# Kernel optimization log

Hardware: AMD Instinct MI355X
Metric: run time of the kernel (lower is better)

The kernel has to match this reference:

```python
import jax, jax.numpy as jnp
import numpy as np

NUM_HEADS = 4
NUM_GROUPS = 32
EPS = 1e-6


def group_norm(x, gamma, beta):
    # x: [b, c, h, w]
    b, c, h, w = x.shape
    xg = x.reshape(b, NUM_GROUPS, c // NUM_GROUPS, h, w)
    mu = xg.mean(axis=(2, 3, 4), keepdims=True)
    var = xg.var(axis=(2, 3, 4), keepdims=True)
    xn = ((xg - mu) * jax.lax.rsqrt(var + EPS)).reshape(b, c, h, w)
    return xn * gamma[None, :, None, None] + beta[None, :, None, None]


def conv1x1(x, W, b):
    # 1x1 conv == per-pixel channel matmul. W: [out_c, in_c], b: [out_c]
    return jnp.einsum('bchw,oc->bohw', x, W) + b[None, :, None, None]


def setup_inputs() -> dict:
    key = jax.random.key(0)
    ks = jax.random.split(key, 8)
    c = 256
    b, h, w = 1, 64, 64
    s = 1.0 / np.sqrt(c)
    return {
        'x_kv': jax.random.normal(ks[0], (b, c, h, w), dtype=jnp.float32),
        'gn_gamma': jnp.ones((c,), dtype=jnp.float32),
        'gn_beta': jnp.zeros((c,), dtype=jnp.float32),
        'Wq': jax.random.normal(ks[1], (c, c), dtype=jnp.float32) * s,
        'bq': jnp.zeros((c,), dtype=jnp.float32),
        'Wk': jax.random.normal(ks[2], (c, c), dtype=jnp.float32) * s,
        'bk': jnp.zeros((c,), dtype=jnp.float32),
        'Wv': jax.random.normal(ks[3], (c, c), dtype=jnp.float32) * s,
        'bv': jnp.zeros((c,), dtype=jnp.float32),
        'Wp': jax.random.normal(ks[4], (c, c), dtype=jnp.float32) * s,
        'bp': jnp.zeros((c,), dtype=jnp.float32),
    }


def reference(x_kv, gn_gamma, gn_beta, Wq, bq, Wk, bk, Wv, bv, Wp, bp):
    b, c, h, w = x_kv.shape
    hd = c // NUM_HEADS
    n = h * w

    h_norm = group_norm(x_kv, gn_gamma, gn_beta)  # self-attn: same norm for q,k,v

    q = conv1x1(h_norm, Wq, bq).reshape(b, NUM_HEADS, hd, n).transpose(0, 1, 3, 2)  # [b,H,n,hd]
    k = conv1x1(h_norm, Wk, bk).reshape(b, NUM_HEADS, hd, n)                        # [b,H,hd,n]
    v = conv1x1(h_norm, Wv, bv).reshape(b, NUM_HEADS, hd, n).transpose(0, 1, 3, 2)  # [b,H,n,hd]

    scores = jnp.einsum('bhnd,bhdm->bhnm', q, k) * (hd ** -0.5)  # [b,H,n,n]
    attn = jax.nn.softmax(scores, axis=-1)
    out = jnp.einsum('bhnm,bhmd->bhnd', attn, v)  # [b,H,n,hd]

    # Faithful to torch: permute(0,2,1,3).contiguous().view(b,c,h,w)
    out = out.transpose(0, 2, 1, 3).reshape(b, c, h, w)
    return x_kv + conv1x1(out, Wp, bp)
```

## Files before the change

### kernel.cpp

```cpp
#include <hip/hip_runtime.h>
#include <hip/hip_bf16.h>

#define NPIX 4096
#define CCH  256
#define HD   64
#define GSIZE 32768

typedef __bf16 bf16x8 __attribute__((ext_vector_type(8)));
typedef __bf16 bf16x4 __attribute__((ext_vector_type(4)));
typedef float  f32x4  __attribute__((ext_vector_type(4)));

#define XPITCH 264


__global__ __launch_bounds__(256) void stats_wconv(
    const float* __restrict__ X,
    const float* __restrict__ Wq, const float* __restrict__ Wk,
    const float* __restrict__ Wv, const float* __restrict__ Wp,
    float* __restrict__ psum, float* __restrict__ pssq, __bf16* __restrict__ Wb)
{
    const int bid = blockIdx.x, t = threadIdx.x;
    if (bid < 256) {
        const float* base = X + bid * 4096;
        float sum = 0.f, ssq = 0.f;
        #pragma unroll
        for (int k = 0; k < 4; ++k) {
            float4 v = *(const float4*)(base + t * 4 + k * 1024);
            sum += v.x + v.y + v.z + v.w;
            ssq += v.x * v.x + v.y * v.y + v.z * v.z + v.w * v.w;
        }
        #pragma unroll
        for (int off = 1; off < 64; off <<= 1) {
            sum += __shfl_xor(sum, off);
            ssq += __shfl_xor(ssq, off);
        }
        __shared__ float red[2][4];
        const int wv = t >> 6;
        if ((t & 63) == 0) { red[0][wv] = sum; red[1][wv] = ssq; }
        __syncthreads();
        if (t == 0) {
            psum[bid] = red[0][0] + red[0][1] + red[0][2] + red[0][3];
            pssq[bid] = red[1][0] + red[1][1] + red[1][2] + red[1][3];
        }
    } else {
        const int j0 = (bid - 256) * 4096 + t * 16;
        const int m  = j0 >> 16;
        const float* W = (m == 0) ? Wq : (m == 1) ? Wk : (m == 2) ? Wv : Wp;
        const float sc = (m == 0) ? 0.125f : 1.f;
        const int off = j0 & 65535;
        #pragma unroll
        for (int k = 0; k < 4; ++k) {
            float4 v = *(const float4*)(W + off + k * 4);
            bf16x4 o;
            o[0] = (__bf16)(v.x * sc); o[1] = (__bf16)(v.y * sc);
            o[2] = (__bf16)(v.z * sc); o[3] = (__bf16)(v.w * sc);
            *(bf16x4*)(Wb + m * 65536 + off + k * 4) = o;
        }
    }
}

__global__ __launch_bounds__(256) void gn_qkv(
    const float* __restrict__ X, const float* __restrict__ gamma,
    const float* __restrict__ beta,
    const float* __restrict__ psum, const float* __restrict__ pssq,
    const __bf16* __restrict__ Wb,
    const float* __restrict__ bq, const float* __restrict__ bk,
    const float* __restrict__ bv,
    __bf16* __restrict__ Qb, __bf16* __restrict__ Kb, __bf16* __restrict__ Vb)
{
    __shared__ __bf16 tile[64 * XPITCH];
    __shared__ float al[256], bl[256];

    const int t = threadIdx.x, lane = t & 63, wave = t >> 6;
    const int l16 = lane & 15, quad = lane >> 4;
    const int p0 = blockIdx.x * 64;
    const int z = blockIdx.y >> 1, och = blockIdx.y & 1;

    {
        const int g = t >> 3;
        float s = 0.f, q = 0.f;
        #pragma unroll
        for (int j = 0; j < 8; ++j) { s += psum[g * 8 + j]; q += pssq[g * 8 + j]; }
        const float mu  = s * (1.f / GSIZE);
        const float var = q * (1.f / GSIZE) - mu * mu;
        const float a = gamma[t] * rsqrtf(var + 1e-6f);
        al[t] = a;
        bl[t] = beta[t] - mu * a;
    }
    __syncthreads();

    #pragma unroll 4
    for (int i = 0; i < 16; ++i) {
        const int c4 = wave * 64 + i * 4;
        f32x4 a4 = *(const f32x4*)(al + c4);
        f32x4 b4 = *(const f32x4*)(bl + c4);
        bf16x4 pk;
        pk[0] = (__bf16)(X[(c4 + 0) * NPIX + p0 + lane] * a4[0] + b4[0]);
        pk[1] = (__bf16)(X[(c4 + 1) * NPIX + p0 + lane] * a4[1] + b4[1]);
        pk[2] = (__bf16)(X[(c4 + 2) * NPIX + p0 + lane] * a4[2] + b4[2]);
        pk[3] = (__bf16)(X[(c4 + 3) * NPIX + p0 + lane] * a4[3] + b4[3]);
        *(bf16x4*)(tile + lane * XPITCH + c4) = pk;
    }
    __syncthreads();

    const int pw = wave * 16;
    bf16x8 xf[8];
    #pragma unroll
    for (int kc = 0; kc < 8; ++kc)
        xf[kc] = *(const bf16x8*)(tile + (pw + l16) * XPITCH + kc * 32 + quad * 8);

    const __bf16* Wz = Wb + z * 65536;
    const float* bias = (z == 0) ? bq : (z == 1) ? bk : bv;

    if (z < 2) {
        const float qs = (z == 0) ? 0.125f : 1.f;
        __bf16* dst = (z == 0) ? Qb : Kb;
        #pragma unroll
        for (int grp = 0; grp < 2; ++grp) {
            f32x4 acc[4] = {};
            #pragma unroll
            for (int kc = 0; kc < 8; ++kc) {
                #pragma unroll
                for (int u = 0; u < 4; ++u) {
                    bf16x8 wf = *(const bf16x8*)(Wz + (och * 128 + (grp * 4 + u) * 16 + l16) * CCH + kc * 32 + quad * 8);
                    acc[u] = __builtin_amdgcn_mfma_f32_16x16x32_bf16(wf, xf[kc], acc[u], 0, 0, 0);
                }
            }
            #pragma unroll
            for (int u = 0; u < 4; ++u) {
                const int ot = och * 8 + grp * 4 + u;
                f32x4 bz = *(const f32x4*)(bias + och * 128 + (grp * 4 + u) * 16 + quad * 4);
                bf16x4 o;
                o[0] = (__bf16)(acc[u][0] + bz[0] * qs);
                o[1] = (__bf16)(acc[u][1] + bz[1] * qs);
                o[2] = (__bf16)(acc[u][2] + bz[2] * qs);
                o[3] = (__bf16)(acc[u][3] + bz[3] * qs);
                const int head = ot >> 2, dloc = (ot & 3) * 16 + quad * 4;
                *(bf16x4*)(dst + head * (NPIX * HD) + (p0 + pw + l16) * HD + dloc) = o;
            }
        }
    } else {
        #pragma unroll
        for (int grp = 0; grp < 2; ++grp) {
            f32x4 acc[4] = {};
            #pragma unroll
            for (int kc = 0; kc < 8; ++kc) {
                #pragma unroll
                for (int u = 0; u < 4; ++u) {
                    bf16x8 wf = *(const bf16x8*)(Wz + (och * 128 + (grp * 4 + u) * 16 + l16) * CCH + kc * 32 + quad * 8);
                    acc[u] = __builtin_amdgcn_mfma_f32_16x16x32_bf16(xf[kc], wf, acc[u], 0, 0, 0);
                }
            }
            #pragma unroll
            for (int u = 0; u < 4; ++u) {
                const int oc = och * 128 + (grp * 4 + u) * 16 + l16;
                const float bz = bias[oc];
                bf16x4 o;
                o[0] = (__bf16)(acc[u][0] + bz); o[1] = (__bf16)(acc[u][1] + bz);
                o[2] = (__bf16)(acc[u][2] + bz); o[3] = (__bf16)(acc[u][3] + bz);
                *(bf16x4*)(Vb + oc * NPIX + p0 + pw + quad * 4) = o;
            }
        }
    }
}

#define KPITCH 72
#define VPITCH 136
#define PPIT   40
#define KBUF   (128 * KPITCH)
#define VBUF   (64 * VPITCH)
#define OFF_K  0
#define OFF_V  (2 * KBUF * 2)
#define OFF_P  (OFF_V + 2 * VBUF * 2)
#define SMEMSZ (OFF_P + 4 * 64 * PPIT * 2)

__global__ __launch_bounds__(256, 1) void attn_mfma(
    const __bf16* __restrict__ Qb, const __bf16* __restrict__ Kb,
    const __bf16* __restrict__ Vb, __bf16* __restrict__ Sb)
{
    __shared__ __align__(16) char smem[SMEMSZ];
    __bf16* ktls = (__bf16*)(smem + OFF_K);
    __bf16* vtls = (__bf16*)(smem + OFF_V);
    __bf16* ptls = (__bf16*)(smem + OFF_P);
    float*  co   = (float*)smem;
    float*  cl   = (float*)(smem + 69632);

    const int t = threadIdx.x, lane = t & 63, wave = t >> 6;
    const int l16 = lane & 15, quad = lane >> 4;

    const int bid  = blockIdx.x;
    const int head = (bid & 7) >> 1;
    const int qt   = ((bid >> 3) << 1) | (bid & 1);
    const int p0   = qt * 64;

    const __bf16* Qh = Qb + head * (NPIX * HD);
    const __bf16* Kh = Kb + head * (NPIX * HD);
    const __bf16* Vh = Vb + head * (HD * NPIX);

    bf16x8 qf[4][2];
    #pragma unroll
    for (int rt = 0; rt < 4; ++rt) {
        const __bf16* qp = Qh + (p0 + rt * 16 + l16) * HD + quad * 8;
        qf[rt][0] = *(const bf16x8*)(qp);
        qf[rt][1] = *(const bf16x8*)(qp + 32);
    }

    bf16x8 ones;
    #pragma unroll
    for (int j = 0; j < 8; ++j) ones[j] = (__bf16)1.0f;

    f32x4 l_acc[4] = {};
    f32x4 o_acc[4][4] = {};

    __bf16* ptw = ptls + wave * (64 * PPIT);

    bf16x8 kpre[4], vpre[4];
    #pragma unroll
    for (int i = 0; i < 4; ++i) {
        const int c = t + 256 * i;
        kpre[i] = *(const bf16x8*)(Kh + (c >> 3) * HD + (c & 7) * 8);
        vpre[i] = *(const bf16x8*)(Vh + (c >> 4) * NPIX + (c & 15) * 8);
    }

    for (int it = 0; it < 32; ++it) {
        const int b = it & 1;
        __bf16* ktb = ktls + b * KBUF;
        __bf16* vtb = vtls + b * VBUF;

        #pragma unroll
        for (int i = 0; i < 4; ++i) {
            const int c = t + 256 * i;
            *(bf16x8*)(ktb + (c >> 3) * KPITCH + (c & 7) * 8)  = kpre[i];
            *(bf16x8*)(vtb + (c >> 4) * VPITCH + (c & 15) * 8) = vpre[i];
        }
        __syncthreads();

        if (it < 31) {
            const int kb = (it + 1) * 128;
            #pragma unroll
            for (int i = 0; i < 4; ++i) {
                const int c = t + 256 * i;
                kpre[i] = *(const bf16x8*)(Kh + (kb + (c >> 3)) * HD + (c & 7) * 8);
                vpre[i] = *(const bf16x8*)(Vh + (c >> 4) * NPIX + kb + (c & 15) * 8);
            }
        }

        bf16x8 kf[2][2], vf[4];
        #pragma unroll
        for (int kt = 0; kt < 2; ++kt) {
            const __bf16* kp = ktb + (wave * 32 + kt * 16 + l16) * KPITCH + quad * 8;
            kf[kt][0] = *(const bf16x8*)(kp);
            kf[kt][1] = *(const bf16x8*)(kp + 32);
        }
        #pragma unroll
        for (int dt = 0; dt < 4; ++dt)
            vf[dt] = *(const bf16x8*)(vtb + (dt * 16 + l16) * VPITCH + wave * 32 + quad * 8);

        f32x4 st[2][4] = {};
        #pragma unroll
        for (int kt = 0; kt < 2; ++kt)
            #pragma unroll
            for (int rt = 0; rt < 4; ++rt) {
                st[kt][rt] = __builtin_amdgcn_mfma_f32_16x16x32_bf16(kf[kt][0], qf[rt][0], st[kt][rt], 0, 0, 0);
                st[kt][rt] = __builtin_amdgcn_mfma_f32_16x16x32_bf16(kf[kt][1], qf[rt][1], st[kt][rt], 0, 0, 0);
            }

        #pragma unroll
        for (int kt = 0; kt < 2; ++kt)
            #pragma unroll
            for (int rt = 0; rt < 4; ++rt) {
                bf16x4 p;
                p[0] = (__bf16)__expf(st[kt][rt][0]);
                p[1] = (__bf16)__expf(st[kt][rt][1]);
                p[2] = (__bf16)__expf(st[kt][rt][2]);
                p[3] = (__bf16)__expf(st[kt][rt][3]);
                *(bf16x4*)(ptw + (rt * 16 + l16) * PPIT + kt * 16 + quad * 4) = p;
            }

        bf16x8 bp[4];
        #pragma unroll
        for (int rt = 0; rt < 4; ++rt)
            bp[rt] = *(const bf16x8*)(ptw + (rt * 16 + l16) * PPIT + quad * 8);

        #pragma unroll
        for (int rt = 0; rt < 4; ++rt)
            l_acc[rt] = __builtin_amdgcn_mfma_f32_16x16x32_bf16(ones, bp[rt], l_acc[rt], 0, 0, 0);

        #pragma unroll
        for (int dt = 0; dt < 4; ++dt)
            #pragma unroll
            for (int rt = 0; rt < 4; ++rt)
                o_acc[dt][rt] = __builtin_amdgcn_mfma_f32_16x16x32_bf16(vf[dt], bp[rt], o_acc[dt][rt], 0, 0, 0);
    }

    __syncthreads();

    #pragma unroll
    for (int dt = 0; dt < 4; ++dt)
        #pragma unroll
        for (int rt = 0; rt < 4; ++rt)
            *(f32x4*)(co + wave * 4352 + (rt * 16 + l16) * 68 + dt * 16 + quad * 4) = o_acc[dt][rt];
    if (quad == 0) {
        #pragma unroll
        for (int rt = 0; rt < 4; ++rt)
            cl[wave * 64 + rt * 16 + l16] = l_acc[rt][0];
    }
    __syncthreads();

    {
        const int row = t >> 2, dc = (t & 3) * 16;
        const float l = cl[row] + cl[64 + row] + cl[128 + row] + cl[192 + row];
        const float inv = 1.f / l;
        f32x4 s[4];
        #pragma unroll
        for (int j = 0; j < 4; ++j) {
            s[j] = f32x4{0.f, 0.f, 0.f, 0.f};
            #pragma unroll
            for (int w = 0; w < 4; ++w)
                s[j] += *(const f32x4*)(co + w * 4352 + row * 68 + dc + j * 4);
        }
        bf16x8 o1, o2;
        #pragma unroll
        for (int j = 0; j < 4; ++j) {
            o1[j]     = (__bf16)(s[0][j] * inv);
            o1[j + 4] = (__bf16)(s[1][j] * inv);
            o2[j]     = (__bf16)(s[2][j] * inv);
            o2[j + 4] = (__bf16)(s[3][j] * inv);
        }
        __bf16* dst = Sb + (p0 + row) * CCH + head * HD + dc;
        *(bf16x8*)(dst)     = o1;
        *(bf16x8*)(dst + 8) = o2;
    }
}

__global__ __launch_bounds__(256) void gemm_proj(
    const __bf16* __restrict__ Sb, const __bf16* __restrict__ Wpb,
    const float* __restrict__ bias, const float* __restrict__ X,
    float* __restrict__ Out)
{
    __shared__ __bf16 Bs[32 * XPITCH];

    const int t = threadIdx.x, lane = t & 63, wave = t >> 6;
    const int l16 = lane & 15, quad = lane >> 4;
    const int p0  = blockIdx.x * 32;
    const int och = blockIdx.y;

    #pragma unroll
    for (int pg = 0; pg < 4; ++pg) {
        bf16x8 v = *(const bf16x8*)(Sb + t * NPIX + p0 + pg * 8);
        #pragma unroll
        for (int j = 0; j < 8; ++j)
            Bs[(pg * 8 + j) * XPITCH + t] = v[j];
    }
    __syncthreads();

    const int pixset = wave & 1, ocset = wave >> 1;
    bf16x8 af[8];
    #pragma unroll
    for (int kc = 0; kc < 8; ++kc)
        af[kc] = *(const bf16x8*)(Bs + (pixset * 16 + l16) * XPITCH + kc * 32 + quad * 8);

    #pragma unroll
    for (int u = 0; u < 4; ++u) {
        f32x4 acc = {};
        const int oc_t = och * 128 + ocset * 64 + u * 16;
        #pragma unroll
        for (int kc = 0; kc < 8; ++kc) {
            bf16x8 wf = *(const bf16x8*)(Wpb + (oc_t + l16) * CCH + kc * 32 + quad * 8);
            acc = __builtin_amdgcn_mfma_f32_16x16x32_bf16(af[kc], wf, acc, 0, 0, 0);
        }
        const int oc  = oc_t + l16;
        const int pix = p0 + pixset * 16 + quad * 4;
        const float bz = bias[oc];
        f32x4 r4 = *(const f32x4*)(X + oc * NPIX + pix);
        f32x4 y;
        y[0] = acc[0] + bz + r4[0];
        y[1] = acc[1] + bz + r4[1];
        y[2] = acc[2] + bz + r4[2];
        y[3] = acc[3] + bz + r4[3];
        *(f32x4*)(Out + oc * NPIX + pix) = y;
    }
}

extern "C" void kernel_launch(void* const* d_in, const int* in_sizes, int n_in,
                              void* d_out, int out_size, void* d_ws, size_t ws_size,
                              hipStream_t stream)
{
    const float* x     = (const float*)d_in[0];
    const float* gamma = (const float*)d_in[1];
    const float* beta  = (const float*)d_in[2];
    const float* Wq    = (const float*)d_in[3];
    const float* bq    = (const float*)d_in[4];
    const float* Wk    = (const float*)d_in[5];
    const float* bk    = (const float*)d_in[6];
    const float* Wv    = (const float*)d_in[7];
    const float* bv    = (const float*)d_in[8];
    const float* Wp    = (const float*)d_in[9];
    const float* bp    = (const float*)d_in[10];
    float* out = (float*)d_out;

    char* ws = (char*)d_ws;
    float*  psum = (float*)(ws);
    float*  pssq = (float*)(ws + 1024);
    __bf16* Wb   = (__bf16*)(ws + 65536);
    __bf16* Qb   = (__bf16*)(ws + (1 << 20));
    __bf16* Kb   = (__bf16*)(ws + (3 << 20));
    __bf16* Vb   = (__bf16*)(ws + (5 << 20));
    __bf16* Sb   = (__bf16*)(ws + (7 << 20));

    stats_wconv<<<320, 256, 0, stream>>>(x, Wq, Wk, Wv, Wp, psum, pssq, Wb);

    dim3 gq(64, 6);
    gn_qkv<<<gq, 256, 0, stream>>>(x, gamma, beta, psum, pssq, Wb,
                                   bq, bk, bv, Qb, Kb, Vb);

    attn_mfma<<<256, 256, 0, stream>>>(Qb, Kb, Vb, Sb);

    dim3 gp(128, 2);
    gemm_proj<<<gp, 256, 0, stream>>>(Sb, Wb + 3 * 65536, bp, x, out);
}
```

Measured before the change: 150.7 us.

## Load K/V fragments directly to registers and shuffle P via permlane swaps

The attention kernel no longer stages K and V tiles through double-buffered shared memory with block-wide barriers. Each wave now loads its own K/V MFMA fragments straight from global memory into registers, using a two-deep register prefetch. The exponentiated score tile is rearranged into the PV operand layout with v_permlane32/16_swap instructions instead of a round trip through LDS. This removes the LDS traffic and __syncthreads from the inner loop. In exchange, each wave issues more uncoalesced global loads of K/V, whose reuse now depends on L2/L1 caching rather than block-shared tiles.

Measured after the change: 140.5 us. 6.8% less time.

```diff
diff --git a/kernel.cpp b/kernel.cpp
--- a/kernel.cpp
+++ b/kernel.cpp
@@ -8,10 +8,20 @@
 
 typedef __bf16 bf16x8 __attribute__((ext_vector_type(8)));
 typedef __bf16 bf16x4 __attribute__((ext_vector_type(4)));
+typedef __bf16 bf16x2 __attribute__((ext_vector_type(2)));
 typedef float  f32x4  __attribute__((ext_vector_type(4)));
+typedef unsigned int uint32x4 __attribute__((ext_vector_type(4)));
 
 #define XPITCH 264
 
+
+__device__ __forceinline__ unsigned pack_bf16x2(float lo, float hi)
+{
+    bf16x2 v;
+    v[0] = (__bf16)lo;
+    v[1] = (__bf16)hi;
+    return __builtin_bit_cast(unsigned, v);
+}
 
 __global__ __launch_bounds__(256) void stats_wconv(
     const float* __restrict__ X,
@@ -164,26 +174,12 @@
     }
 }
 
-#define KPITCH 72
-#define VPITCH 136
-#define PPIT   40
-#define KBUF   (128 * KPITCH)
-#define VBUF   (64 * VPITCH)
-#define OFF_K  0
-#define OFF_V  (2 * KBUF * 2)
-#define OFF_P  (OFF_V + 2 * VBUF * 2)
-#define SMEMSZ (OFF_P + 4 * 64 * PPIT * 2)
-
 __global__ __launch_bounds__(256, 1) void attn_mfma(
     const __bf16* __restrict__ Qb, const __bf16* __restrict__ Kb,
     const __bf16* __restrict__ Vb, __bf16* __restrict__ Sb)
 {
-    __shared__ __align__(16) char smem[SMEMSZ];
-    __bf16* ktls = (__bf16*)(smem + OFF_K);
-    __bf16* vtls = (__bf16*)(smem + OFF_V);
-    __bf16* ptls = (__bf16*)(smem + OFF_P);
-    float*  co   = (float*)smem;
-    float*  cl   = (float*)(smem + 69632);
+    __shared__ __align__(16) float co[4 * 64 * 68];
+    __shared__ float cl[4 * 64];
 
     const int t = threadIdx.x, lane = t & 63, wave = t >> 6;
     const int l16 = lane & 15, quad = lane >> 4;
@@ -194,8 +190,8 @@
     const int p0   = qt * 64;
 
     const __bf16* Qh = Qb + head * (NPIX * HD);
-    const __bf16* Kh = Kb + head * (NPIX * HD);
-    const __bf16* Vh = Vb + head * (HD * NPIX);
+    const __bf16* Kh = Kb + head * (NPIX * HD) + (wave * 32 + l16) * HD + quad * 8;
+    const __bf16* Vh = Vb + head * (HD * NPIX) + l16 * NPIX + wave * 32 + quad * 8;
 
     bf16x8 qf[4][2];
     #pragma unroll
@@ -212,88 +208,56 @@
     f32x4 l_acc[4] = {};
     f32x4 o_acc[4][4] = {};
 
-    __bf16* ptw = ptls + wave * (64 * PPIT);
-
-    bf16x8 kpre[4], vpre[4];
-    #pragma unroll
-    for (int i = 0; i < 4; ++i) {
-        const int c = t + 256 * i;
-        kpre[i] = *(const bf16x8*)(Kh + (c >> 3) * HD + (c & 7) * 8);
-        vpre[i] = *(const bf16x8*)(Vh + (c >> 4) * NPIX + (c & 15) * 8);
-    }
-
-    for (int it = 0; it < 32; ++it) {
-        const int b = it & 1;
-        __bf16* ktb = ktls + b * KBUF;
-        __bf16* vtb = vtls + b * VBUF;
-
-        #pragma unroll
-        for (int i = 0; i < 4; ++i) {
-            const int c = t + 256 * i;
-            *(bf16x8*)(ktb + (c >> 3) * KPITCH + (c & 7) * 8)  = kpre[i];
-            *(bf16x8*)(vtb + (c >> 4) * VPITCH + (c & 15) * 8) = vpre[i];
-        }
-        __syncthreads();
-
-        if (it < 31) {
-            const int kb = (it + 1) * 128;
-            #pragma unroll
-            for (int i = 0; i < 4; ++i) {
-                const int c = t + 256 * i;
-                kpre[i] = *(const bf16x8*)(Kh + (kb + (c >> 3)) * HD + (c & 7) * 8);
-                vpre[i] = *(const bf16x8*)(Vh + (c >> 4) * NPIX + kb + (c & 15) * 8);
-            }
-        }
-
-        bf16x8 kf[2][2], vf[4];
-        #pragma unroll
-        for (int kt = 0; kt < 2; ++kt) {
-            const __bf16* kp = ktb + (wave * 32 + kt * 16 + l16) * KPITCH + quad * 8;
-            kf[kt][0] = *(const bf16x8*)(kp);
-            kf[kt][1] = *(const bf16x8*)(kp + 32);
-        }
+    auto ldKV = [&](int it, bf16x8 (&kf)[2][2], bf16x8 (&vf)[4]) {
+        const __bf16* kp = Kh + it * (128 * HD);
+        kf[0][0] = *(const bf16x8*)(kp);
+        kf[0][1] = *(const bf16x8*)(kp + 32);
+        kf[1][0] = *(const bf16x8*)(kp + 16 * HD);
+        kf[1][1] = *(const bf16x8*)(kp + 16 * HD + 32);
+        const __bf16* vp = Vh + it * 128;
         #pragma unroll
         for (int dt = 0; dt < 4; ++dt)
-            vf[dt] = *(const bf16x8*)(vtb + (dt * 16 + l16) * VPITCH + wave * 32 + quad * 8);
-
-        f32x4 st[2][4] = {};
-        #pragma unroll
-        for (int kt = 0; kt < 2; ++kt)
-            #pragma unroll
-            for (int rt = 0; rt < 4; ++rt) {
-                st[kt][rt] = __builtin_amdgcn_mfma_f32_16x16x32_bf16(kf[kt][0], qf[rt][0], st[kt][rt], 0, 0, 0);
-                st[kt][rt] = __builtin_amdgcn_mfma_f32_16x16x32_bf16(kf[kt][1], qf[rt][1], st[kt][rt], 0, 0, 0);
-            }
-
-        #pragma unroll
-        for (int kt = 0; kt < 2; ++kt)
-            #pragma unroll
-            for (int rt = 0; rt < 4; ++rt) {
-                bf16x4 p;
-                p[0] = (__bf16)__expf(st[kt][rt][0]);
-                p[1] = (__bf16)__expf(st[kt][rt][1]);
-                p[2] = (__bf16)__expf(st[kt][rt][2]);
-                p[3] = (__bf16)__expf(st[kt][rt][3]);
-                *(bf16x4*)(ptw + (rt * 16 + l16) * PPIT + kt * 16 + quad * 4) = p;
-            }
-
-        bf16x8 bp[4];
-        #pragma unroll
-        for (int rt = 0; rt < 4; ++rt)
-            bp[rt] = *(const bf16x8*)(ptw + (rt * 16 + l16) * PPIT + quad * 8);
-
-        #pragma unroll
-        for (int rt = 0; rt < 4; ++rt)
-            l_acc[rt] = __builtin_amdgcn_mfma_f32_16x16x32_bf16(ones, bp[rt], l_acc[rt], 0, 0, 0);
-
-        #pragma unroll
-        for (int dt = 0; dt < 4; ++dt)
-            #pragma unroll
-            for (int rt = 0; rt < 4; ++rt)
-                o_acc[dt][rt] = __builtin_amdgcn_mfma_f32_16x16x32_bf16(vf[dt], bp[rt], o_acc[dt][rt], 0, 0, 0);
-    }
-
-    __syncthreads();
+            vf[dt] = *(const bf16x8*)(vp + dt * (16 * NPIX));
+    };
+
+    auto step = [&](const bf16x8 (&kf)[2][2], const bf16x8 (&vf)[4]) {
+        f32x4 st0[4] = {}, st1[4] = {};
+        #pragma unroll
+        for (int rt = 0; rt < 4; ++rt) {
+            st0[rt] = __builtin_amdgcn_mfma_f32_16x16x32_bf16(kf[0][0], qf[rt][0], st0[rt], 0, 0, 0);
+            st0[rt] = __builtin_amdgcn_mfma_f32_16x16x32_bf16(kf[0][1], qf[rt][1], st0[rt], 0, 0, 0);
+            st1[rt] = __builtin_amdgcn_mfma_f32_16x16x32_bf16(kf[1][0], qf[rt][0], st1[rt], 0, 0, 0);
+            st1[rt] = __builtin_amdgcn_mfma_f32_16x16x32_bf16(kf[1][1], qf[rt][1], st1[rt], 0, 0, 0);
+        }
+        #pragma unroll
+        for (int rt = 0; rt < 4; ++rt) {
+            unsigned a0 = pack_bf16x2(__expf(st0[rt][0]), __expf(st0[rt][1]));
+            unsigned a1 = pack_bf16x2(__expf(st0[rt][2]), __expf(st0[rt][3]));
+            unsigned b0 = pack_bf16x2(__expf(st1[rt][0]), __expf(st1[rt][1]));
+            unsigned b1 = pack_bf16x2(__expf(st1[rt][2]), __expf(st1[rt][3]));
+            asm("v_permlane32_swap_b32 %0, %1" : "+v"(a0), "+v"(b0));
+            asm("v_permlane32_swap_b32 %0, %1" : "+v"(a1), "+v"(b1));
+            asm("v_permlane16_swap_b32 %0, %1" : "+v"(a0), "+v"(b0));
+            asm("v_permlane16_swap_b32 %0, %1" : "+v"(a1), "+v"(b1));
+            uint32x4 w;
+            w[0] = a0; w[1] = a1; w[2] = b0; w[3] = b1;
+            const bf16x8 bp = __builtin_bit_cast(bf16x8, w);
+            l_acc[rt] = __builtin_amdgcn_mfma_f32_16x16x32_bf16(ones, bp, l_acc[rt], 0, 0, 0);
+            #pragma unroll
+            for (int dt = 0; dt < 4; ++dt)
+                o_acc[dt][rt] = __builtin_amdgcn_mfma_f32_16x16x32_bf16(vf[dt], bp, o_acc[dt][rt], 0, 0, 0);
+        }
+    };
+
+    bf16x8 ka[2][2], va[4], kb[2][2], vb[4];
+    ldKV(0, ka, va);
+    #pragma unroll 1
+    for (int it = 0; it < 32; it += 2) {
+        ldKV(it + 1, kb, vb);
+        step(ka, va);
+        if (it + 2 < 32) ldKV(it + 2, ka, va);
+        step(kb, vb);
+    }
 
     #pragma unroll
     for (int dt = 0; dt < 4; ++dt)
```
